# Performance work log

Hardware: AMD Instinct MI355X
Metric: run time of the kernel (lower is better)

Reference implementation:

```python
import jax, jax.numpy as jnp
import numpy as np

BIG = jnp.float32(1e30)  # stands in for +inf without inf-arithmetic issues


def _pairwise_euclidean(x, y):
    # x: [N, d], y: [M, d] -> [N, M] Euclidean distances (scipy cdist default)
    sq = (jnp.sum(x * x, axis=1)[:, None]
          + jnp.sum(y * y, axis=1)[None, :]
          - 2.0 * (x @ y.T))
    return jnp.sqrt(jnp.maximum(sq, 1e-12))


def _minplus_combine(e1, e2):
    # elements represent affine-tropical maps f(v) = min(m, v + s); compose f2 o f1
    m1, s1 = e1
    m2, s2 = e2
    return (jnp.minimum(m2, m1 + s2), s1 + s2)


def _dtw_distance(x, y):
    """dtw-python default: symmetric2 step pattern, unnormalized distance.

    D[0,0] = c[0,0]; D[0,j] = D[0,j-1] + c[0,j]; D[i,0] = D[i-1,0] + c[i,0]
    D[i,j] = min(D[i-1,j-1] + 2*c[i,j], D[i-1,j] + c[i,j], D[i,j-1] + c[i,j])
    """
    c = _pairwise_euclidean(x, y)  # [N, M]
    row0 = jnp.cumsum(c[0])        # first row: only horizontal steps

    def row_step(Dp, crow):
        # Dp: D[i-1, :]; within-row recurrence D[j] = min(b[j], D[j-1] + c[j])
        shift = jnp.concatenate([jnp.full((1,), BIG, crow.dtype), Dp[:-1]])
        b = jnp.minimum(shift + 2.0 * crow, Dp + crow)
        # min-plus prefix scan (tropical semiring), log-depth & vectorized
        m, _ = jax.lax.associative_scan(_minplus_combine, (b, crow))
        return m, ()

    Dlast, _ = jax.lax.scan(row_step, row0, c[1:])
    return Dlast[-1]


def setup_inputs() -> dict:
    key = jax.random.key(0)
    kx, ky = jax.random.split(key)
    N, M, d = 4096, 4096, 64
    x = jax.random.normal(kx, (N, d), dtype=jnp.float32)
    y = jax.random.normal(ky, (M, d), dtype=jnp.float32)
    return {"x": x, "y": y}


def reference(x, y):
    return _dtw_distance(x, y)
```

## Files before the change

kernel.cpp:

```cpp
#include <hip/hip_runtime.h>
#include <stdint.h>

#define N4K 4096
#define BIGF 1e30f
#define POIS 0xAAAAAAAAu

typedef __attribute__((address_space(1))) unsigned as1_u32;
typedef __attribute__((address_space(3))) unsigned as3_u32;

__device__ __forceinline__ void gl_lds4(const float* g, float* l) {
  __builtin_amdgcn_global_load_lds((as1_u32*)(uintptr_t)g,
                                   (as3_u32*)(uint32_t)(uintptr_t)l, 4, 0, 0);
}

__device__ __forceinline__ float dpp_shr1(float oldv, float src) {
  int r = __builtin_amdgcn_update_dpp(__float_as_int(oldv), __float_as_int(src),
                                      0x138 , 0xF, 0xF, false);
  return __int_as_float(r);
}

__device__ __forceinline__ void st_bnd(unsigned* p, float v) {
  __hip_atomic_store(p, __float_as_uint(v), __ATOMIC_RELAXED,
                     __HIP_MEMORY_SCOPE_AGENT);
}
__device__ __forceinline__ unsigned ld_bnd(const unsigned* p) {
  return __hip_atomic_load((unsigned*)p, __ATOMIC_RELAXED,
                           __HIP_MEMORY_SCOPE_AGENT);
}

__global__ void k_poison(unsigned* __restrict__ bnd) {
  bnd[(size_t)blockIdx.x * 256 + threadIdx.x] = POIS;
}

__global__ __launch_bounds__(256) void k_cost(const float* __restrict__ X,
                                              const float* __restrict__ Y,
                                              float* __restrict__ ct) {
  __shared__ __align__(16) float ys[64][132];
  __shared__ __align__(16) float xs[64][132];
  __shared__ float ynm[128];
  __shared__ float xnm[128];
  const int tid = threadIdx.x;
  const int jt = blockIdx.y << 7;
  const int it = blockIdx.x << 7;
#pragma unroll
  for (int r = 0; r < 32; ++r) {
    int e = tid + (r << 8);
    int row = e >> 6, k = e & 63;
    ys[k][row] = Y[(size_t)(jt + row) * 64 + k];
    xs[k][row] = X[(size_t)(it + row) * 64 + k];
  }
  __syncthreads();
  {
    int r = tid & 127;
    float s = 0.f;
    if (tid < 128) {
#pragma unroll
      for (int k = 0; k < 64; ++k) { float v = ys[k][r]; s = fmaf(v, v, s); }
      ynm[r] = s;
    } else {
#pragma unroll
      for (int k = 0; k < 64; ++k) { float v = xs[k][r]; s = fmaf(v, v, s); }
      xnm[r] = s;
    }
  }
  __syncthreads();
  const int tx = tid & 15, ty = tid >> 4;
  float acc[8][8];
#pragma unroll
  for (int r = 0; r < 8; ++r)
#pragma unroll
    for (int c = 0; c < 8; ++c) acc[r][c] = 0.f;
#pragma unroll 4
  for (int k = 0; k < 64; ++k) {
    float a[8], b[8];
    *(float4*)&a[0] = *(const float4*)&ys[k][(ty << 2)];
    *(float4*)&a[4] = *(const float4*)&ys[k][64 + (ty << 2)];
    *(float4*)&b[0] = *(const float4*)&xs[k][(tx << 2)];
    *(float4*)&b[4] = *(const float4*)&xs[k][64 + (tx << 2)];
#pragma unroll
    for (int r = 0; r < 8; ++r)
#pragma unroll
      for (int c = 0; c < 8; ++c) acc[r][c] = fmaf(a[r], b[c], acc[r][c]);
  }
#pragma unroll
  for (int r = 0; r < 8; ++r) {
    const int lr = ((r & 4) << 4) + (ty << 2) + (r & 3);
    const float yn = ynm[lr];
    float o[8];
#pragma unroll
    for (int c = 0; c < 8; ++c) {
      const int lc = ((c & 4) << 4) + (tx << 2) + (c & 3);
      float sq = yn + xnm[lc] - 2.f * acc[r][c];
      o[c] = sqrtf(fmaxf(sq, 1e-12f));
    }
    float* dst = ct + (size_t)(jt + lr) * N4K + it;
    *(float4*)(dst + (tx << 2)) = make_float4(o[0], o[1], o[2], o[3]);
    *(float4*)(dst + 64 + (tx << 2)) = make_float4(o[4], o[5], o[6], o[7]);
  }
}

template <bool DO_NXTQ, bool PRED>
__device__ __forceinline__ void run_iter(const float* tl, const float* topb,
                                         int ubb, float (&curc)[16],
                                         float4 (&curq)[4], float (&nxtc)[16],
                                         float4 (&nxtq)[4], float& d,
                                         float& eprev, int lane, bool is00,
                                         bool doSt, unsigned* bdst) {
  const int nub = ubb + 16;
  const float* ba = tl + (((nub - lane) & 255) << 6) + lane;
#pragma unroll
  for (int s = 0; s < 16; ++s) nxtc[s] = ba[s << 6];
  if (DO_NXTQ) {
#pragma unroll
    for (int q = 0; q < 4; ++q)
      nxtq[q] = *(const float4*)&topb[(nub + (q << 2)) & 127];
  }
  float g0 = 0.f, g1 = 0.f, g2v = 0.f, g3 = 0.f;
#pragma unroll
  for (int s = 0; s < 16; ++s) {
    const int u = ubb + s;
    const float cst = curc[s];
    const float cnx = (s < 15) ? curc[s + 1] : nxtc[0];
    const float4 qq = curq[s >> 2];
    const float tqe = ((s & 3) == 0)   ? qq.x
                      : ((s & 3) == 1) ? qq.y
                      : ((s & 3) == 2) ? qq.z
                                       : qq.w;
    float n1 = dpp_shr1(tqe, d);
    float dn = fminf(fminf(n1, d), eprev) + cst;
    if (PRED) {
      if (is00 && u == 0) dn = cst;
      if ((unsigned)(u - lane) > 4095u) dn = d;
    }
    eprev = n1 + cnx;
    d = dn;
    if ((s & 3) == 0) g0 = d;
    if ((s & 3) == 1) g1 = d;
    if ((s & 3) == 2) g2v = d;
    if ((s & 3) == 3) {
      g3 = d;
      if (doSt) {
        const int jb = u - 66;
        if (PRED) {
          if ((unsigned)(jb + 0) <= 4095u) st_bnd(bdst + (jb + 0), g0);
          if ((unsigned)(jb + 1) <= 4095u) st_bnd(bdst + (jb + 1), g1);
          if ((unsigned)(jb + 2) <= 4095u) st_bnd(bdst + (jb + 2), g2v);
          if ((unsigned)(jb + 3) <= 4095u) st_bnd(bdst + (jb + 3), g3);
        } else {
          st_bnd(bdst + (jb + 0), g0);
          st_bnd(bdst + (jb + 1), g1);
          st_bnd(bdst + (jb + 2), g2v);
          st_bnd(bdst + (jb + 3), g3);
        }
      }
    }
  }
}

__global__ __launch_bounds__(64) void k_dp(const float* __restrict__ ct,
                                           unsigned* __restrict__ bnd,
                                           float* __restrict__ out) {
  __shared__ __align__(16) float tl[272 * 64];
  __shared__ __align__(16) float topb[128];
  const int lane = threadIdx.x;
  const int b = (int)blockIdx.x;
  const int strip = ((b & 7) << 3) | (b >> 3);
  const int i0 = strip << 6;
  const bool hasTop = (strip != 0);
  const bool doSt = (strip != 63) && (lane == 63);
  const bool is00 = (strip == 0) && (lane == 0);
  const unsigned* bsrc = bnd + (size_t)(hasTop ? strip - 1 : 0) * N4K;
  unsigned* bdst = bnd + (size_t)strip * N4K;

  auto stage = [&](int m) {
    const float* gb = ct + (size_t)(m << 6) * N4K + i0 + lane;
    float* wb = tl + ((m & 3) << 12) + lane;
#pragma unroll
    for (int r = 0; r < 64; ++r) gl_lds4(gb + (size_t)r * N4K, wb + (r << 6));
    if ((m & 3) == 0) {
      float* wm = tl + (256 << 6) + lane;
#pragma unroll
      for (int r = 0; r < 16; ++r) gl_lds4(gb + (size_t)r * N4K, wm + (r << 6));
    }
  };

  unsigned tvP = 0, tvN = 0;
  if (hasTop) tvP = ld_bnd(bsrc + lane);
  stage(0);
  stage(1);
  if (hasTop) {
    int gc = 0;
    while (__any((int)(tvP == POIS)) && ++gc < (1 << 16))
      tvP = ld_bnd(bsrc + lane);
    topb[lane] = __uint_as_float(tvP);
  } else {
    topb[lane] = BIGF;
    topb[64 + lane] = BIGF;
  }
  asm volatile("s_waitcnt vmcnt(0)" ::: "memory");

  float cA[16], cB[16];
  float4 qA[4], qB[4];
  {
    const float* ba0 = tl + (((0 - lane) & 255) << 6) + lane;
#pragma unroll
    for (int s = 0; s < 16; ++s) cA[s] = ba0[s << 6];
  }
#pragma unroll
  for (int q = 0; q < 4; ++q) qA[q] = *(const float4*)&topb[(q << 2)];

  float d = BIGF, eprev = BIGF;

  auto pollQ = [&](int q, int n) {
    int gc = 0;
    while (__any((int)((lane >> 4) == q && tvP == POIS)) && ++gc < (1 << 16))
      tvP = ld_bnd(bsrc + (n << 6) + lane);
    if ((lane >> 4) == q) topb[((n & 1) << 6) + lane] = __uint_as_float(tvP);
  };

#pragma unroll 1
  for (int n = 0; n <= 64; ++n) {
    const bool doTv = hasTop && (n + 1 <= 63);
    if (doTv) tvN = ld_bnd(bsrc + ((n + 1) << 6) + lane);
    if (n + 2 <= 63) stage(n + 2);
    const bool doQ = hasTop && (n <= 63);
    const int ub = n << 6;
    if (doQ) pollQ(1, n);
    if (n == 0 || n == 64) {
      run_iter<true, true>(tl, topb, ub + 0, cA, qA, cB, qB, d, eprev, lane,
                           is00, doSt, bdst);
      if (doQ) pollQ(2, n);
      run_iter<true, true>(tl, topb, ub + 16, cB, qB, cA, qA, d, eprev, lane,
                           is00, doSt, bdst);
      if (doQ) pollQ(3, n);
      run_iter<true, true>(tl, topb, ub + 32, cA, qA, cB, qB, d, eprev, lane,
                           is00, doSt, bdst);
      run_iter<false, true>(tl, topb, ub + 48, cB, qB, cA, qA, d, eprev, lane,
                            is00, doSt, bdst);
    } else {
      run_iter<true, false>(tl, topb, ub + 0, cA, qA, cB, qB, d, eprev, lane,
                            is00, doSt, bdst);
      if (doQ) pollQ(2, n);
      run_iter<true, false>(tl, topb, ub + 16, cB, qB, cA, qA, d, eprev, lane,
                            is00, doSt, bdst);
      if (doQ) pollQ(3, n);
      run_iter<true, false>(tl, topb, ub + 32, cA, qA, cB, qB, d, eprev, lane,
                            is00, doSt, bdst);
      run_iter<false, false>(tl, topb, ub + 48, cB, qB, cA, qA, d, eprev, lane,
                             is00, doSt, bdst);
    }
    if (doTv) {
      int gc = 0;
      while (__any((int)((lane >> 4) == 0 && tvN == POIS)) && ++gc < (1 << 16))
        tvN = ld_bnd(bsrc + ((n + 1) << 6) + lane);
      if ((lane >> 4) == 0)
        topb[(((n + 1) & 1) << 6) + lane] = __uint_as_float(tvN);
      tvP = tvN;
    }
#pragma unroll
    for (int q = 0; q < 4; ++q)
      qA[q] = *(const float4*)&topb[((ub + 64) + (q << 2)) & 127];
  }
  if (strip == 63 && lane == 63) out[0] = d;
}

extern "C" void kernel_launch(void* const* d_in, const int* in_sizes, int n_in,
                              void* d_out, int out_size, void* d_ws,
                              size_t ws_size, hipStream_t stream) {
  (void)in_sizes; (void)n_in; (void)out_size; (void)ws_size;
  const float* X = (const float*)d_in[0];
  const float* Y = (const float*)d_in[1];
  float* out = (float*)d_out;
  float* ct = (float*)d_ws;
  unsigned* bnd = (unsigned*)((char*)d_ws + (size_t)N4K * N4K * sizeof(float));

  k_poison<<<1024, 256, 0, stream>>>(bnd);
  k_cost<<<dim3(32, 32), 256, 0, stream>>>(X, Y, ct);
  k_dp<<<64, 64, 0, stream>>>(ct, bnd, out);
}
```

Baseline: 976.4 us.

## Replace LDS-direct loads with register-staged software pipeline for cost tiles

Swaps the global_load_lds direct-to-LDS staging of cost-matrix chunks for a four-buffer register pipeline. Each quarter iteration issues global loads into one register buffer and writes a previously loaded buffer to LDS. This drops the block-wide vmcnt(0) wait and spreads loads across the compute steps. It also adds an initial poll of the second boundary chunk. The cost is 64 extra VGPRs of staging and explicit LDS write instructions, which may lengthen the serial DP critical path.

Result: slower. 1.053 ms (+7.9%).

```diff
diff --git a/kernel.cpp b/kernel.cpp
--- a/kernel.cpp
+++ b/kernel.cpp
@@ -4,14 +4,6 @@
 #define N4K 4096
 #define BIGF 1e30f
 #define POIS 0xAAAAAAAAu
-
-typedef __attribute__((address_space(1))) unsigned as1_u32;
-typedef __attribute__((address_space(3))) unsigned as3_u32;
-
-__device__ __forceinline__ void gl_lds4(const float* g, float* l) {
-  __builtin_amdgcn_global_load_lds((as1_u32*)(uintptr_t)g,
-                                   (as3_u32*)(uint32_t)(uintptr_t)l, 4, 0, 0);
-}
 
 __device__ __forceinline__ float dpp_shr1(float oldv, float src) {
   int r = __builtin_amdgcn_update_dpp(__float_as_int(oldv), __float_as_int(src),
@@ -172,32 +164,49 @@
   const unsigned* bsrc = bnd + (size_t)(hasTop ? strip - 1 : 0) * N4K;
   unsigned* bdst = bnd + (size_t)strip * N4K;
 
-  auto stage = [&](int m) {
-    const float* gb = ct + (size_t)(m << 6) * N4K + i0 + lane;
-    float* wb = tl + ((m & 3) << 12) + lane;
-#pragma unroll
-    for (int r = 0; r < 64; ++r) gl_lds4(gb + (size_t)r * N4K, wb + (r << 6));
-    if ((m & 3) == 0) {
+  float bufA[16], bufB[16], bufC[16], bufD[16];
+
+  auto loadB = [&](float (&buf)[16], int a) {
+    const float* gb = ct + i0 + lane;
+#pragma unroll
+    for (int r = 0; r < 16; ++r) {
+      int j = (a << 4) + r;
+      j = j > N4K - 1 ? N4K - 1 : j;
+      buf[r] = gb[(size_t)j * N4K];
+    }
+  };
+  auto writeB = [&](float (&buf)[16], int a) {
+    float* wb = tl + (((a << 4) & 255) << 6) + lane;
+#pragma unroll
+    for (int r = 0; r < 16; ++r) wb[r << 6] = buf[r];
+    if (((a << 4) & 255) == 0) {
       float* wm = tl + (256 << 6) + lane;
 #pragma unroll
-      for (int r = 0; r < 16; ++r) gl_lds4(gb + (size_t)r * N4K, wm + (r << 6));
+      for (int r = 0; r < 16; ++r) wm[r << 6] = buf[r];
     }
   };
 
   unsigned tvP = 0, tvN = 0;
   if (hasTop) tvP = ld_bnd(bsrc + lane);
-  stage(0);
-  stage(1);
+  loadB(bufA, 0);
+  loadB(bufB, 1);
+  loadB(bufC, 2);
+  loadB(bufD, 3);
+  writeB(bufA, 0);
+  writeB(bufB, 1);
   if (hasTop) {
     int gc = 0;
     while (__any((int)(tvP == POIS)) && ++gc < (1 << 16))
       tvP = ld_bnd(bsrc + lane);
     topb[lane] = __uint_as_float(tvP);
+    unsigned t2 = ld_bnd(bsrc + 64 + lane);
+    gc = 0;
+    while (__any((int)(t2 == POIS)) && ++gc < (1 << 16))
+      t2 = ld_bnd(bsrc + 64 + lane);
   } else {
     topb[lane] = BIGF;
     topb[64 + lane] = BIGF;
   }
-  asm volatile("s_waitcnt vmcnt(0)" ::: "memory");
 
   float cA[16], cB[16];
   float4 qA[4], qB[4];
@@ -220,32 +229,46 @@
 
 #pragma unroll 1
   for (int n = 0; n <= 64; ++n) {
+    const int m0 = n << 2;
     const bool doTv = hasTop && (n + 1 <= 63);
     if (doTv) tvN = ld_bnd(bsrc + ((n + 1) << 6) + lane);
-    if (n + 2 <= 63) stage(n + 2);
     const bool doQ = hasTop && (n <= 63);
     const int ub = n << 6;
+    loadB(bufA, m0 + 4);
+    writeB(bufC, m0 + 2);
     if (doQ) pollQ(1, n);
     if (n == 0 || n == 64) {
       run_iter<true, true>(tl, topb, ub + 0, cA, qA, cB, qB, d, eprev, lane,
                            is00, doSt, bdst);
+      loadB(bufB, m0 + 5);
+      writeB(bufD, m0 + 3);
       if (doQ) pollQ(2, n);
       run_iter<true, true>(tl, topb, ub + 16, cB, qB, cA, qA, d, eprev, lane,
                            is00, doSt, bdst);
+      loadB(bufC, m0 + 6);
+      writeB(bufA, m0 + 4);
       if (doQ) pollQ(3, n);
       run_iter<true, true>(tl, topb, ub + 32, cA, qA, cB, qB, d, eprev, lane,
                            is00, doSt, bdst);
+      loadB(bufD, m0 + 7);
+      writeB(bufB, m0 + 5);
       run_iter<false, true>(tl, topb, ub + 48, cB, qB, cA, qA, d, eprev, lane,
                             is00, doSt, bdst);
     } else {
       run_iter<true, false>(tl, topb, ub + 0, cA, qA, cB, qB, d, eprev, lane,
                             is00, doSt, bdst);
+      loadB(bufB, m0 + 5);
+      writeB(bufD, m0 + 3);
       if (doQ) pollQ(2, n);
       run_iter<true, false>(tl, topb, ub + 16, cB, qB, cA, qA, d, eprev, lane,
                             is00, doSt, bdst);
+      loadB(bufC, m0 + 6);
+      writeB(bufA, m0 + 4);
       if (doQ) pollQ(3, n);
       run_iter<true, false>(tl, topb, ub + 32, cA, qA, cB, qB, d, eprev, lane,
                             is00, doSt, bdst);
+      loadB(bufD, m0 + 7);
+      writeB(bufB, m0 + 5);
       run_iter<false, false>(tl, topb, ub + 48, cB, qB, cA, qA, d, eprev, lane,
                              is00, doSt, bdst);
     }
```
